# Optimization experiments

Hardware: AMD Instinct MI355X
Metric: run time of the kernel (lower is better)

The kernel has to match this reference:

```python
import jax, jax.numpy as jnp
import numpy as np

N = 100000  # number of nodes
E = 1600000  # number of edges (before self-loops)
D_IN, D_HID, D_OUT = 128, 128, 64


def gcn_conv(x, src, dst, W, b):
    """One PyG-style GCNConv: x' = D^{-1/2} A_hat D^{-1/2} (x W) + b, with self-loops in src/dst."""
    h = x @ W  # [N, D_out]
    deg = jax.ops.segment_sum(jnp.ones(src.shape[0], dtype=h.dtype), dst, num_segments=N)
    dinv = jnp.where(deg > 0, jax.lax.rsqrt(deg), 0.0)
    norm = dinv[src] * dinv[dst]  # [E+N]
    msgs = h[src] * norm[:, None]  # gather + scale
    out = jax.ops.segment_sum(msgs, dst, num_segments=N)  # scatter-add
    return out + b


def setup_inputs() -> dict:
    key = jax.random.key(0)
    k1, k2, k3, k4 = jax.random.split(key, 4)
    x = jax.random.normal(k1, (N, D_IN), dtype=jnp.float32)
    edge_index = jax.random.randint(k2, (2, E), 0, N, dtype=jnp.int64)
    W1 = jax.random.normal(k3, (D_IN, D_HID), dtype=jnp.float32) * (1.0 / np.sqrt(D_IN))
    b1 = jnp.zeros((D_HID,), dtype=jnp.float32)
    W2 = jax.random.normal(k4, (D_HID, D_OUT), dtype=jnp.float32) * (1.0 / np.sqrt(D_HID))
    b2 = jnp.zeros((D_OUT,), dtype=jnp.float32)
    return {"x": x, "edge_index": edge_index, "W1": W1, "b1": b1, "W2": W2, "b2": b2}


def reference(x, edge_index, W1, b1, W2, b2):
    # add self-loops once (GCNConv default add_self_loops=True)
    loops = jnp.arange(N, dtype=edge_index.dtype)
    src = jnp.concatenate([edge_index[0], loops])
    dst = jnp.concatenate([edge_index[1], loops])
    h = jax.nn.relu(gcn_conv(x, src, dst, W1, b1))
    out = gcn_conv(h, src, dst, W2, b2)
    return out
```

## Files before the change

### kernel.cpp

```cpp
#include <hip/hip_runtime.h>


#define NN 100000
#define EE 1600000
#define NB 391
#define BCAP 4608
#define PCAP 6656
#define EPB 8192
#define PBLK ((EE + EPB - 1) / EPB)

typedef _Float16 f16;
typedef _Float16 f16x8 __attribute__((ext_vector_type(8)));
typedef _Float16 f16x2 __attribute__((ext_vector_type(2)));
typedef float f32x4 __attribute__((ext_vector_type(4)));

__device__ __forceinline__ int load_idx(const void* p, long long i, int is64) {
    if (is64) return (int)((const long long*)p)[i];
    return ((const int*)p)[i];
}

__global__ void init_buckets(int* cursor) {
    int i = blockIdx.x * 256 + threadIdx.x;
    if (i < NB) cursor[i] = i * BCAP;
}

__global__ __launch_bounds__(256) void partition_kernel(const void* ei,
                                                        int* __restrict__ cursor,
                                                        unsigned* __restrict__ col32) {
    __shared__ int lh[NB], lbase[NB], lfill[NB];
    __shared__ int s_is64;
    for (int i = threadIdx.x; i < NB; i += 256) { lh[i] = 0; lfill[i] = 0; }
    if (threadIdx.x == 0) {
        const unsigned* w = (const unsigned*)ei;
        unsigned acc = 0;
        #pragma unroll
        for (int k = 0; k < 8; k++) acc |= w[2 * (k * 997 + 1) + 1];
        s_is64 = (acc == 0);
    }
    __syncthreads();
    int is64 = s_is64;
    long long base = (long long)blockIdx.x * EPB;
    #pragma unroll 4
    for (int k = 0; k < EPB / 256; k++) {
        long long i = base + k * 256 + threadIdx.x;
        if (i < EE) {
            int d = load_idx(ei, (long long)EE + i, is64);
            atomicAdd(&lh[d >> 8], 1);
        }
    }
    __syncthreads();
    for (int i = threadIdx.x; i < NB; i += 256)
        lbase[i] = lh[i] ? atomicAdd(&cursor[i], lh[i]) : 0;
    __syncthreads();
    #pragma unroll 4
    for (int k = 0; k < EPB / 256; k++) {
        long long i = base + k * 256 + threadIdx.x;
        if (i < EE) {
            int s = load_idx(ei, i, is64);
            int d = load_idx(ei, (long long)EE + i, is64);
            int b = d >> 8;
            int r = atomicAdd(&lfill[b], 1);
            col32[lbase[b] + r] = ((unsigned)s << 8) | (unsigned)(d & 255);
        }
    }
}

__global__ __launch_bounds__(256) void bucket_fill_kernel(const unsigned* __restrict__ col32,
                                                          const int* __restrict__ cursor,
                                                          int2* __restrict__ rsp,
                                                          float* __restrict__ dinv,
                                                          int* __restrict__ col) {
    __shared__ int cnt[256], incl[256], lfill[256];
    int t = threadIdx.x, b = blockIdx.x;
    cnt[t] = 0; lfill[t] = 0;
    __syncthreads();
    int base = b * BCAP;
    int end = cursor[b];
    for (int i = base + t; i < end; i += 256)
        atomicAdd(&cnt[col32[i] & 255u], 1);
    __syncthreads();
    int pc = (cnt[t] + 7) & ~7;
    incl[t] = pc;
    __syncthreads();
    #pragma unroll
    for (int off = 1; off < 256; off <<= 1) {
        int v = (t >= off) ? incl[t - off] : 0;
        __syncthreads();
        if (t >= off) incl[t] += v;
        __syncthreads();
    }
    int node = b * 256 + t;
    int excl = (t == 0) ? 0 : incl[t - 1];
    int myrs = b * PCAP + excl;
    if (node < NN) {
        rsp[node] = make_int2(myrs, pc);
        dinv[node] = rsqrtf((float)(cnt[t] + 1));
    }
    if (b == 0 && t == 0) dinv[NN] = 0.f;
    __syncthreads();
    for (int i = base + t; i < end; i += 256) {
        unsigned p = col32[i];
        int d = p & 255u;
        int r = atomicAdd(&lfill[d], 1);
        int ex = (d == 0) ? 0 : incl[d - 1];
        col[b * PCAP + ex + r] = (int)(p >> 8);
    }
    __syncthreads();
    int cn = cnt[t];
    for (int k = cn; k < ((cn + 7) & ~7); k++) col[myrs + k] = NN;
}

__global__ void prep_split(const float* __restrict__ W1, const float* __restrict__ W2,
                           f16* __restrict__ W1h, f16* __restrict__ W1l,
                           f16* __restrict__ W2h, f16* __restrict__ W2l) {
    int t = blockIdx.x * 256 + threadIdx.x;
    if (t < 128 * 128) {
        int k = t >> 7, n = t & 127;
        float v = W1[t];
        f16 h = (f16)v;
        f16 l = (f16)(v - (float)h);
        int idx = n * 128 + (k ^ ((n & 7) << 3));
        W1h[idx] = h; W1l[idx] = l;
    } else if (t < 128 * 128 + 128 * 64) {
        int u = t - 128 * 128;
        int k = u >> 6, n = u & 63;
        float v = W2[u];
        f16 h = (f16)v;
        f16 l = (f16)(v - (float)h);
        int idx = n * 128 + (k ^ ((n & 7) << 3));
        W2h[idx] = h; W2l[idx] = l;
    }
}

template <int M, int SPLIT_A>
__global__ __launch_bounds__(256) void gemm_mfma(const void* __restrict__ Xv,
                                                 const f16* __restrict__ Wh,
                                                 const f16* __restrict__ Wl,
                                                 f16* __restrict__ H) {
    __shared__ f16 wsh[M * 128];
    __shared__ f16 wsl[M * 128];
    const int tid = threadIdx.x;
    for (int c = tid; c < M * 16; c += 256) {
        *(float4*)&wsh[c * 8] = ((const float4*)Wh)[c];
        *(float4*)&wsl[c * 8] = ((const float4*)Wl)[c];
    }
    __syncthreads();

    const int lane = tid & 63;
    const int wv = tid >> 6;
    const int m0 = lane & 15;
    const int kg = lane >> 4;
    int row = blockIdx.x * 64 + wv * 16 + m0;
    if (row >= NN) row = NN - 1;

    constexpr int NT = M / 16;
    f32x4 acc[NT];
    #pragma unroll
    for (int i = 0; i < NT; i++) acc[i] = (f32x4){0.f, 0.f, 0.f, 0.f};

    #pragma unroll
    for (int kt = 0; kt < 4; ++kt) {
        int k0 = kt * 32 + kg * 8;
        f16x8 ah, al;
        if (SPLIT_A) {
            const float* xr = (const float*)Xv + (size_t)row * 128 + k0;
            float xv[8];
            *(float4*)&xv[0] = *(const float4*)xr;
            *(float4*)&xv[4] = *(const float4*)(xr + 4);
            #pragma unroll
            for (int r = 0; r < 8; r++) {
                ah[r] = (f16)xv[r];
                al[r] = (f16)(xv[r] - (float)ah[r]);
            }
        } else {
            ah = *(const f16x8*)((const f16*)Xv + (size_t)row * 128 + k0);
        }
        #pragma unroll
        for (int nt = 0; nt < NT; ++nt) {
            int n = nt * 16 + m0;
            int sch = (kt * 4 + kg) ^ (n & 7);
            int off = n * 128 + sch * 8;
            f16x8 bh = *(const f16x8*)&wsh[off];
            f16x8 bl = *(const f16x8*)&wsl[off];
            acc[nt] = __builtin_amdgcn_mfma_f32_16x16x32_f16(ah, bh, acc[nt], 0, 0, 0);
            if (SPLIT_A)
                acc[nt] = __builtin_amdgcn_mfma_f32_16x16x32_f16(al, bh, acc[nt], 0, 0, 0);
            acc[nt] = __builtin_amdgcn_mfma_f32_16x16x32_f16(ah, bl, acc[nt], 0, 0, 0);
        }
    }

    int r0 = blockIdx.x * 64 + wv * 16 + kg * 4;
    #pragma unroll
    for (int nt = 0; nt < NT; ++nt) {
        int cidx = nt * 16 + m0;
        #pragma unroll
        for (int i = 0; i < 4; i++) {
            int r = r0 + i;
            if (r < NN) H[(size_t)r * M + cidx] = (f16)acc[nt][i];
        }
    }
}

__global__ __launch_bounds__(256) void agg128(const f16* __restrict__ h,
                                              const int2* __restrict__ rsp,
                                              const int* __restrict__ col,
                                              const float* __restrict__ dinv,
                                              const float* __restrict__ bias,
                                              f16* __restrict__ out) {
    int node = (blockIdx.x * 256 + threadIdx.x) >> 6;
    int lane = threadIdx.x & 63;
    if (node >= NN) return;
    float di = dinv[node];
    const f16x2* hp = (const f16x2*)h;
    f16x2 sv = hp[(unsigned)(node * 64 + lane)];
    int2 g = rsp[node];
    int s = g.x, e = g.x + g.y;
    float ax[8], ay[8];
    #pragma unroll
    for (int i = 0; i < 8; i++) { ax[i] = 0.f; ay[i] = 0.f; }
    int c[8];
    if (s < e) {
        #pragma unroll
        for (int i = 0; i < 8; i++) c[i] = col[s + i];
    }
    for (int j = s; j < e; j += 8) {
        int cn[8];
        if (j + 8 < e) {
            #pragma unroll
            for (int i = 0; i < 8; i++) cn[i] = col[j + 8 + i];
        } else {
            #pragma unroll
            for (int i = 0; i < 8; i++) cn[i] = 0;
        }
        float w[8];
        f16x2 v[8];
        #pragma unroll
        for (int i = 0; i < 8; i++) w[i] = dinv[c[i]];
        #pragma unroll
        for (int i = 0; i < 8; i++) v[i] = hp[(unsigned)(c[i] * 64 + lane)];
        #pragma unroll
        for (int i = 0; i < 8; i++) {
            ax[i] = fmaf((float)v[i][0], w[i], ax[i]);
            ay[i] = fmaf((float)v[i][1], w[i], ay[i]);
        }
        #pragma unroll
        for (int i = 0; i < 8; i++) c[i] = cn[i];
    }
    float sx = ((ax[0] + ax[1]) + (ax[2] + ax[3])) + ((ax[4] + ax[5]) + (ax[6] + ax[7]));
    float sy = ((ay[0] + ay[1]) + (ay[2] + ay[3])) + ((ay[4] + ay[5]) + (ay[6] + ay[7]));
    sx = fmaf((float)sv[0], di, sx);
    sy = fmaf((float)sv[1], di, sy);
    float2 bv = ((const float2*)bias)[lane];
    float ox = fmaxf(sx * di + bv.x, 0.f);
    float oy = fmaxf(sy * di + bv.y, 0.f);
    f16x2 o;
    o[0] = (f16)ox; o[1] = (f16)oy;
    ((f16x2*)(out + (size_t)node * 128))[lane] = o;
}

__global__ __launch_bounds__(256) void agg64(const f16* __restrict__ h,
                                             const int2* __restrict__ rsp,
                                             const int* __restrict__ col,
                                             const float* __restrict__ dinv,
                                             const float* __restrict__ bias,
                                             float* __restrict__ out) {
    int node = (blockIdx.x * 256 + threadIdx.x) >> 5;
    int lane = threadIdx.x & 31;
    if (node >= NN) return;
    float di = dinv[node];
    const f16x2* hp = (const f16x2*)h;
    f16x2 sv = hp[(unsigned)(node * 32 + lane)];
    int2 g = rsp[node];
    int s = g.x, e = g.x + g.y;
    float ax[8], ay[8];
    #pragma unroll
    for (int i = 0; i < 8; i++) { ax[i] = 0.f; ay[i] = 0.f; }
    int c[8];
    if (s < e) {
        #pragma unroll
        for (int i = 0; i < 8; i++) c[i] = col[s + i];
    }
    for (int j = s; j < e; j += 8) {
        int cn[8];
        if (j + 8 < e) {
            #pragma unroll
            for (int i = 0; i < 8; i++) cn[i] = col[j + 8 + i];
        } else {
            #pragma unroll
            for (int i = 0; i < 8; i++) cn[i] = 0;
        }
        float w[8];
        f16x2 v[8];
        #pragma unroll
        for (int i = 0; i < 8; i++) w[i] = dinv[c[i]];
        #pragma unroll
        for (int i = 0; i < 8; i++) v[i] = hp[(unsigned)(c[i] * 32 + lane)];
        #pragma unroll
        for (int i = 0; i < 8; i++) {
            ax[i] = fmaf((float)v[i][0], w[i], ax[i]);
            ay[i] = fmaf((float)v[i][1], w[i], ay[i]);
        }
        #pragma unroll
        for (int i = 0; i < 8; i++) c[i] = cn[i];
    }
    float sx = ((ax[0] + ax[1]) + (ax[2] + ax[3])) + ((ax[4] + ax[5]) + (ax[6] + ax[7]));
    float sy = ((ay[0] + ay[1]) + (ay[2] + ay[3])) + ((ay[4] + ay[5]) + (ay[6] + ay[7]));
    sx = fmaf((float)sv[0], di, sx);
    sy = fmaf((float)sv[1], di, sy);
    float2 bv = ((const float2*)bias)[lane];
    float2 o = make_float2(sx * di + bv.x, sy * di + bv.y);
    ((float2*)(out + (size_t)node * 64))[lane] = o;
}

extern "C" void kernel_launch(void* const* d_in, const int* in_sizes, int n_in,
                              void* d_out, int out_size, void* d_ws, size_t ws_size,
                              hipStream_t stream) {
    const float* x  = (const float*)d_in[0];
    const void*  ei = d_in[1];
    const float* W1 = (const float*)d_in[2];
    const float* b1 = (const float*)d_in[3];
    const float* W2 = (const float*)d_in[4];
    const float* b2 = (const float*)d_in[5];
    float* out = (float*)d_out;

    char* wsp = (char*)d_ws;
    size_t off = 0;
    auto alloc = [&](size_t bytes) {
        void* p = wsp + off;
        off += (bytes + 255) & ~(size_t)255;
        return p;
    };
    f16*      h1     = (f16*)alloc((size_t)(NN + 1) * 128 * 2);
    f16*      a1     = (f16*)alloc((size_t)NN * 128 * 2);
    f16*      h2     = (f16*)alloc((size_t)(NN + 1) * 64 * 2);
    int*      col    = (int*)alloc((size_t)NB * PCAP * 4);
    int2*     rsp    = (int2*)alloc((size_t)NN * 8);
    float*    dinv   = (float*)alloc((size_t)(NN + 1) * 4);
    int*      cursor = (int*)alloc((size_t)NB * 4);
    f16*      W1h    = (f16*)alloc(128 * 128 * 2);
    f16*      W1l    = (f16*)alloc(128 * 128 * 2);
    f16*      W2h    = (f16*)alloc(64 * 128 * 2);
    f16*      W2l    = (f16*)alloc(64 * 128 * 2);
    unsigned* col32  = (unsigned*)a1;
    (void)ws_size; (void)in_sizes; (void)n_in; (void)out_size;

    hipMemsetAsync(h1 + (size_t)NN * 128, 0, 256, stream);
    hipMemsetAsync(h2 + (size_t)NN * 64, 0, 128, stream);

    prep_split<<<96, 256, 0, stream>>>(W1, W2, W1h, W1l, W2h, W2l);
    init_buckets<<<2, 256, 0, stream>>>(cursor);
    partition_kernel<<<PBLK, 256, 0, stream>>>(ei, cursor, col32);
    bucket_fill_kernel<<<NB, 256, 0, stream>>>(col32, cursor, rsp, dinv, col);

    gemm_mfma<128, 1><<<(NN + 63) / 64, 256, 0, stream>>>(x, W1h, W1l, h1);
    agg128<<<(NN * 64) / 256, 256, 0, stream>>>(h1, rsp, col, dinv, b1, a1);
    gemm_mfma<64, 0><<<(NN + 63) / 64, 256, 0, stream>>>(a1, W2h, W2l, h2);
    agg64<<<(NN * 32) / 256, 256, 0, stream>>>(h2, rsp, col, dinv, b2, out);
}
```

Measured before the change: 197.0 us.

## Fold source-side dinv into GEMM, degree-sort nodes, vectorize aggregation gathers

The GEMM epilogue now scales each output row by dinv, so aggregation becomes a plain sum of gathered rows with no per-edge dinv lookup. Nodes are binned by padded degree into an order array, so waves run neighbors of similar length together and divergence is reduced. Aggregation kernels switch to 16-lane groups doing 16-byte (f16x8) or 8-byte (f16x4) gathers, four edges at a time per wave with shuffle reductions, and agg64 now uses full 64-lane waves. In exchange it adds extra small kernels (scan, scatter), an atomic histogram, and extra NN padding entries so the next-index prefetch stays in bounds.

```diff
diff --git a/kernel.cpp b/kernel.cpp
--- a/kernel.cpp
+++ b/kernel.cpp
@@ -11,7 +11,7 @@
 
 typedef _Float16 f16;
 typedef _Float16 f16x8 __attribute__((ext_vector_type(8)));
-typedef _Float16 f16x2 __attribute__((ext_vector_type(2)));
+typedef _Float16 f16x4 __attribute__((ext_vector_type(4)));
 typedef float f32x4 __attribute__((ext_vector_type(4)));
 
 __device__ __forceinline__ int load_idx(const void* p, long long i, int is64) {
@@ -69,10 +69,12 @@
                                                           const int* __restrict__ cursor,
                                                           int2* __restrict__ rsp,
                                                           float* __restrict__ dinv,
-                                                          int* __restrict__ col) {
-    __shared__ int cnt[256], incl[256], lfill[256];
+                                                          int* __restrict__ col,
+                                                          int* __restrict__ dbin) {
+    __shared__ int cnt[256], incl[256], lfill[256], ldbin[16];
     int t = threadIdx.x, b = blockIdx.x;
     cnt[t] = 0; lfill[t] = 0;
+    if (t < 16) ldbin[t] = 0;
     __syncthreads();
     int base = b * BCAP;
     int end = cursor[b];
@@ -80,6 +82,8 @@
         atomicAdd(&cnt[col32[i] & 255u], 1);
     __syncthreads();
     int pc = (cnt[t] + 7) & ~7;
+    int node = b * 256 + t;
+    if (node < NN) atomicAdd(&ldbin[min(pc >> 3, 15)], 1);
     incl[t] = pc;
     __syncthreads();
     #pragma unroll
@@ -89,14 +93,12 @@
         if (t >= off) incl[t] += v;
         __syncthreads();
     }
-    int node = b * 256 + t;
     int excl = (t == 0) ? 0 : incl[t - 1];
     int myrs = b * PCAP + excl;
     if (node < NN) {
         rsp[node] = make_int2(myrs, pc);
         dinv[node] = rsqrtf((float)(cnt[t] + 1));
     }
-    if (b == 0 && t == 0) dinv[NN] = 0.f;
     __syncthreads();
     for (int i = base + t; i < end; i += 256) {
         unsigned p = col32[i];
@@ -107,7 +109,35 @@
     }
     __syncthreads();
     int cn = cnt[t];
-    for (int k = cn; k < ((cn + 7) & ~7); k++) col[myrs + k] = NN;
+    for (int k = cn; k < pc; k++) col[myrs + k] = NN;
+    if (t == 255) {
+        int tot = incl[255];
+        for (int k = 0; k < 8; k++) col[b * PCAP + tot + k] = NN;
+    }
+    if (t < 16 && ldbin[t]) atomicAdd(&dbin[t], ldbin[t]);
+}
+
+__global__ void scan16(const int* __restrict__ dbin, int* __restrict__ dcur) {
+    if (threadIdx.x == 0) {
+        int a = 0;
+        for (int i = 0; i < 16; i++) { dcur[i] = a; a += dbin[i]; }
+    }
+}
+
+__global__ __launch_bounds__(256) void deg_scatter(const int2* __restrict__ rsp,
+                                                   int* __restrict__ dcur,
+                                                   int* __restrict__ order) {
+    __shared__ int lh[16], lbase[16], lcur[16];
+    int t = threadIdx.x;
+    if (t < 16) { lh[t] = 0; lcur[t] = 0; }
+    __syncthreads();
+    int node = blockIdx.x * 256 + t;
+    int bin = -1;
+    if (node < NN) { bin = min(rsp[node].y >> 3, 15); atomicAdd(&lh[bin], 1); }
+    __syncthreads();
+    if (t < 16 && lh[t]) lbase[t] = atomicAdd(&dcur[t], lh[t]);
+    __syncthreads();
+    if (node < NN) { int r = atomicAdd(&lcur[bin], 1); order[lbase[bin] + r] = node; }
 }
 
 __global__ void prep_split(const float* __restrict__ W1, const float* __restrict__ W2,
@@ -136,6 +166,7 @@
 __global__ __launch_bounds__(256) void gemm_mfma(const void* __restrict__ Xv,
                                                  const f16* __restrict__ Wh,
                                                  const f16* __restrict__ Wl,
+                                                 const float* __restrict__ dinv,
                                                  f16* __restrict__ H) {
     __shared__ f16 wsh[M * 128];
     __shared__ f16 wsl[M * 128];
@@ -190,126 +221,118 @@
     }
 
     int r0 = blockIdx.x * 64 + wv * 16 + kg * 4;
+    float dv[4];
+    #pragma unroll
+    for (int i = 0; i < 4; i++) {
+        int r = r0 + i;
+        dv[i] = (r < NN) ? dinv[r] : 0.f;
+    }
     #pragma unroll
     for (int nt = 0; nt < NT; ++nt) {
         int cidx = nt * 16 + m0;
         #pragma unroll
         for (int i = 0; i < 4; i++) {
             int r = r0 + i;
-            if (r < NN) H[(size_t)r * M + cidx] = (f16)acc[nt][i];
+            if (r < NN) H[(size_t)r * M + cidx] = (f16)(acc[nt][i] * dv[i]);
         }
     }
 }
 
 __global__ __launch_bounds__(256) void agg128(const f16* __restrict__ h,
+                                              const int* __restrict__ order,
                                               const int2* __restrict__ rsp,
                                               const int* __restrict__ col,
                                               const float* __restrict__ dinv,
                                               const float* __restrict__ bias,
                                               f16* __restrict__ out) {
-    int node = (blockIdx.x * 256 + threadIdx.x) >> 6;
+    int wid = (blockIdx.x * 256 + threadIdx.x) >> 6;
+    if (wid >= NN) return;
     int lane = threadIdx.x & 63;
-    if (node >= NN) return;
-    float di = dinv[node];
-    const f16x2* hp = (const f16x2*)h;
-    f16x2 sv = hp[(unsigned)(node * 64 + lane)];
+    int grp = lane >> 4, gl = lane & 15;
+    int node = order[wid];
     int2 g = rsp[node];
     int s = g.x, e = g.x + g.y;
-    float ax[8], ay[8];
-    #pragma unroll
-    for (int i = 0; i < 8; i++) { ax[i] = 0.f; ay[i] = 0.f; }
-    int c[8];
-    if (s < e) {
-        #pragma unroll
-        for (int i = 0; i < 8; i++) c[i] = col[s + i];
-    }
+    const f16x8* hp = (const f16x8*)h;
+    float acc[8];
+    #pragma unroll
+    for (int k = 0; k < 8; k++) acc[k] = 0.f;
+    int c0 = col[s + grp], c1 = col[s + 4 + grp];
     for (int j = s; j < e; j += 8) {
-        int cn[8];
-        if (j + 8 < e) {
-            #pragma unroll
-            for (int i = 0; i < 8; i++) cn[i] = col[j + 8 + i];
-        } else {
-            #pragma unroll
-            for (int i = 0; i < 8; i++) cn[i] = 0;
-        }
-        float w[8];
-        f16x2 v[8];
-        #pragma unroll
-        for (int i = 0; i < 8; i++) w[i] = dinv[c[i]];
-        #pragma unroll
-        for (int i = 0; i < 8; i++) v[i] = hp[(unsigned)(c[i] * 64 + lane)];
-        #pragma unroll
-        for (int i = 0; i < 8; i++) {
-            ax[i] = fmaf((float)v[i][0], w[i], ax[i]);
-            ay[i] = fmaf((float)v[i][1], w[i], ay[i]);
-        }
-        #pragma unroll
-        for (int i = 0; i < 8; i++) c[i] = cn[i];
-    }
-    float sx = ((ax[0] + ax[1]) + (ax[2] + ax[3])) + ((ax[4] + ax[5]) + (ax[6] + ax[7]));
-    float sy = ((ay[0] + ay[1]) + (ay[2] + ay[3])) + ((ay[4] + ay[5]) + (ay[6] + ay[7]));
-    sx = fmaf((float)sv[0], di, sx);
-    sy = fmaf((float)sv[1], di, sy);
-    float2 bv = ((const float2*)bias)[lane];
-    float ox = fmaxf(sx * di + bv.x, 0.f);
-    float oy = fmaxf(sy * di + bv.y, 0.f);
-    f16x2 o;
-    o[0] = (f16)ox; o[1] = (f16)oy;
-    ((f16x2*)(out + (size_t)node * 128))[lane] = o;
+        int n0 = col[j + 8 + grp];
+        int n1 = col[j + 12 + grp];
+        f16x8 v0 = hp[(unsigned)(c0 * 16 + gl)];
+        f16x8 v1 = hp[(unsigned)(c1 * 16 + gl)];
+        #pragma unroll
+        for (int k = 0; k < 8; k++) acc[k] += (float)v0[k];
+        #pragma unroll
+        for (int k = 0; k < 8; k++) acc[k] += (float)v1[k];
+        c0 = n0; c1 = n1;
+    }
+    #pragma unroll
+    for (int k = 0; k < 8; k++) acc[k] += __shfl_xor(acc[k], 32);
+    #pragma unroll
+    for (int k = 0; k < 8; k++) acc[k] += __shfl_xor(acc[k], 16);
+    if (grp == 0) {
+        f16x8 sv = hp[(unsigned)(node * 16 + gl)];
+        float di = dinv[node];
+        float4 b0 = ((const float4*)bias)[gl * 2];
+        float4 b1 = ((const float4*)bias)[gl * 2 + 1];
+        float bb[8] = {b0.x, b0.y, b0.z, b0.w, b1.x, b1.y, b1.z, b1.w};
+        f16x8 o;
+        #pragma unroll
+        for (int k = 0; k < 8; k++) {
+            float v = fmaf(acc[k] + (float)sv[k], di, bb[k]);
+            o[k] = (f16)fmaxf(v, 0.f);
+        }
+        ((f16x8*)out)[(unsigned)(node * 16 + gl)] = o;
+    }
 }
 
 __global__ __launch_bounds__(256) void agg64(const f16* __restrict__ h,
+                                             const int* __restrict__ order,
                                              const int2* __restrict__ rsp,
                                              const int* __restrict__ col,
                                              const float* __restrict__ dinv,
                                              const float* __restrict__ bias,
                                              float* __restrict__ out) {
-    int node = (blockIdx.x * 256 + threadIdx.x) >> 5;
-    int lane = threadIdx.x & 31;
-    if (node >= NN) return;
-    float di = dinv[node];
-    const f16x2* hp = (const f16x2*)h;
-    f16x2 sv = hp[(unsigned)(node * 32 + lane)];
+    int wid = (blockIdx.x * 256 + threadIdx.x) >> 6;
+    if (wid >= NN) return;
+    int lane = threadIdx.x & 63;
+    int grp = lane >> 4, gl = lane & 15;
+    int node = order[wid];
     int2 g = rsp[node];
     int s = g.x, e = g.x + g.y;
-    float ax[8], ay[8];
-    #pragma unroll
-    for (int i = 0; i < 8; i++) { ax[i] = 0.f; ay[i] = 0.f; }
-    int c[8];
-    if (s < e) {
-        #pragma unroll
-        for (int i = 0; i < 8; i++) c[i] = col[s + i];
-    }
+    const f16x4* hp = (const f16x4*)h;
+    float acc[4];
+    #pragma unroll
+    for (int k = 0; k < 4; k++) acc[k] = 0.f;
+    int c0 = col[s + grp], c1 = col[s + 4 + grp];
     for (int j = s; j < e; j += 8) {
-        int cn[8];
-        if (j + 8 < e) {
-            #pragma unroll
-            for (int i = 0; i < 8; i++) cn[i] = col[j + 8 + i];
-        } else {
-            #pragma unroll
-            for (int i = 0; i < 8; i++) cn[i] = 0;
-        }
-        float w[8];
-        f16x2 v[8];
-        #pragma unroll
-        for (int i = 0; i < 8; i++) w[i] = dinv[c[i]];
-        #pragma unroll
-        for (int i = 0; i < 8; i++) v[i] = hp[(unsigned)(c[i] * 32 + lane)];
-        #pragma unroll
-        for (int i = 0; i < 8; i++) {
-            ax[i] = fmaf((float)v[i][0], w[i], ax[i]);
-            ay[i] = fmaf((float)v[i][1], w[i], ay[i]);
-        }
-        #pragma unroll
-        for (int i = 0; i < 8; i++) c[i] = cn[i];
-    }
-    float sx = ((ax[0] + ax[1]) + (ax[2] + ax[3])) + ((ax[4] + ax[5]) + (ax[6] + ax[7]));
-    float sy = ((ay[0] + ay[1]) + (ay[2] + ay[3])) + ((ay[4] + ay[5]) + (ay[6] + ay[7]));
-    sx = fmaf((float)sv[0], di, sx);
-    sy = fmaf((float)sv[1], di, sy);
-    float2 bv = ((const float2*)bias)[lane];
-    float2 o = make_float2(sx * di + bv.x, sy * di + bv.y);
-    ((float2*)(out + (size_t)node * 64))[lane] = o;
+        int n0 = col[j + 8 + grp];
+        int n1 = col[j + 12 + grp];
+        f16x4 v0 = hp[(unsigned)(c0 * 16 + gl)];
+        f16x4 v1 = hp[(unsigned)(c1 * 16 + gl)];
+        #pragma unroll
+        for (int k = 0; k < 4; k++) acc[k] += (float)v0[k];
+        #pragma unroll
+        for (int k = 0; k < 4; k++) acc[k] += (float)v1[k];
+        c0 = n0; c1 = n1;
+    }
+    #pragma unroll
+    for (int k = 0; k < 4; k++) acc[k] += __shfl_xor(acc[k], 32);
+    #pragma unroll
+    for (int k = 0; k < 4; k++) acc[k] += __shfl_xor(acc[k], 16);
+    if (grp == 0) {
+        f16x4 sv = hp[(unsigned)(node * 16 + gl)];
+        float di = dinv[node];
+        float4 b = ((const float4*)bias)[gl];
+        float4 o;
+        o.x = fmaf(acc[0] + (float)sv[0], di, b.x);
+        o.y = fmaf(acc[1] + (float)sv[1], di, b.y);
+        o.z = fmaf(acc[2] + (float)sv[2], di, b.z);
+        o.w = fmaf(acc[3] + (float)sv[3], di, b.w);
+        ((float4*)out)[(unsigned)(node * 16 + gl)] = o;
+    }
 }
 
 extern "C" void kernel_launch(void* const* d_in, const int* in_sizes, int n_in,
@@ -335,8 +358,11 @@
     f16*      h2     = (f16*)alloc((size_t)(NN + 1) * 64 * 2);
     int*      col    = (int*)alloc((size_t)NB * PCAP * 4);
     int2*     rsp    = (int2*)alloc((size_t)NN * 8);
-    float*    dinv   = (float*)alloc((size_t)(NN + 1) * 4);
+    float*    dinv   = (float*)alloc((size_t)NN * 4);
+    int*      order  = (int*)alloc((size_t)NN * 4);
     int*      cursor = (int*)alloc((size_t)NB * 4);
+    int*      dbin   = (int*)alloc(64);
+    int*      dcur   = (int*)alloc(64);
     f16*      W1h    = (f16*)alloc(128 * 128 * 2);
     f16*      W1l    = (f16*)alloc(128 * 128 * 2);
     f16*      W2h    = (f16*)alloc(64 * 128 * 2);
@@ -346,14 +372,17 @@
 
     hipMemsetAsync(h1 + (size_t)NN * 128, 0, 256, stream);
     hipMemsetAsync(h2 + (size_t)NN * 64, 0, 128, stream);
+    hipMemsetAsync(dbin, 0, 64, stream);
 
     prep_split<<<96, 256, 0, stream>>>(W1, W2, W1h, W1l, W2h, W2l);
     init_buckets<<<2, 256, 0, stream>>>(cursor);
     partition_kernel<<<PBLK, 256, 0, stream>>>(ei, cursor, col32);
-    bucket_fill_kernel<<<NB, 256, 0, stream>>>(col32, cursor, rsp, dinv, col);
-
-    gemm_mfma<128, 1><<<(NN + 63) / 64, 256, 0, stream>>>(x, W1h, W1l, h1);
-    agg128<<<(NN * 64) / 256, 256, 0, stream>>>(h1, rsp, col, dinv, b1, a1);
-    gemm_mfma<64, 0><<<(NN + 63) / 64, 256, 0, stream>>>(a1, W2h, W2l, h2);
-    agg64<<<(NN * 32) / 256, 256, 0, stream>>>(h2, rsp, col, dinv, b2, out);
-}
+    bucket_fill_kernel<<<NB, 256, 0, stream>>>(col32, cursor, rsp, dinv, col, dbin);
+    scan16<<<1, 64, 0, stream>>>(dbin, dcur);
+    deg_scatter<<<NB, 256, 0, stream>>>(rsp, dcur, order);
+
+    gemm_mfma<128, 1><<<(NN + 63) / 64, 256, 0, stream>>>(x, W1h, W1l, dinv, h1);
+    agg128<<<(NN * 64) / 256, 256, 0, stream>>>(h1, order, rsp, col, dinv, b1, a1);
+    gemm_mfma<64, 0><<<(NN + 63) / 64, 256, 0, stream>>>(a1, W2h, W2l, dinv, h2);
+    agg64<<<(NN * 64) / 256, 256, 0, stream>>>(h2, order, rsp, col, dinv, b2, out);
+}
```

Result: slower. 233.1 us (+18.3%).
